# Performance work log

Measured on AMD Instinct MI355X. Metric: run time of the kernel, lower is better.

Reference implementation:

```python
import jax, jax.numpy as jnp
import numpy as np

B, T, E, H, D = 4, 2048, 1024, 16, 64  # batch, seq(block_size), n_embed, num_heads, hidden_dim


def setup_inputs() -> dict:
    key = jax.random.key(0)
    ks = jax.random.split(key, 10)
    s_in = 1.0 / np.sqrt(E)
    return {
        "x": jax.random.normal(ks[0], (B, T, E), dtype=jnp.float32),
        "Wq": jax.random.normal(ks[1], (H, E, D), dtype=jnp.float32) * s_in,
        "bq": jnp.zeros((H, D), dtype=jnp.float32),
        "Wk": jax.random.normal(ks[2], (H, E, D), dtype=jnp.float32) * s_in,
        "bk": jnp.zeros((H, D), dtype=jnp.float32),
        "Wv": jax.random.normal(ks[3], (H, E, D), dtype=jnp.float32) * s_in,
        "bv": jnp.zeros((H, D), dtype=jnp.float32),
        "Wp": jax.random.normal(ks[4], (E, E), dtype=jnp.float32) * s_in,
        "bp": jnp.zeros((E,), dtype=jnp.float32),
    }


def reference(x, Wq, bq, Wk, bk, Wv, bv, Wp, bp):
    # Batched equivalent of the per-head Python loop: each head h computes
    # causal scaled-dot-product attention with its own Q/K/V projections.
    q = jnp.einsum("bte,hed->bhtd", x, Wq) + bq[None, :, None, :]
    k = jnp.einsum("bte,hed->bhtd", x, Wk) + bk[None, :, None, :]
    v = jnp.einsum("bte,hed->bhtd", x, Wv) + bv[None, :, None, :]
    scale = 1.0 / jnp.sqrt(jnp.asarray(D, dtype=x.dtype))
    scores = jnp.einsum("bhtd,bhsd->bhts", q, k) * scale  # [B,H,T,T]
    causal = jnp.tril(jnp.ones((T, T), dtype=bool))
    scores = jnp.where(causal[None, None, :, :], scores, jnp.asarray(-jnp.inf, dtype=x.dtype))
    att = jax.nn.softmax(scores, axis=-1)
    head_out = jnp.einsum("bhts,bhsd->bhtd", att, v)  # [B,H,T,D]
    # concat heads along last dim: [B,T,H*D] == [B,T,E]
    cat = head_out.transpose(0, 2, 1, 3).reshape(B, T, H * D)
    out = cat @ Wp + bp  # final projection (dropout is identity in eval)
    return out
```

## Files before the change

kernel.cpp:

```cpp
#include <hip/hip_runtime.h>


typedef __attribute__((ext_vector_type(8))) __bf16 bf16x8;
typedef __attribute__((ext_vector_type(4))) float f32x4;
typedef __attribute__((ext_vector_type(16))) float f32x16;
typedef __attribute__((ext_vector_type(4))) unsigned int u32x4;
typedef __attribute__((ext_vector_type(2))) unsigned int u32x2;
typedef unsigned short u16;
typedef unsigned int u32;

#define DEV __device__ __forceinline__

#define QK_SCALE 0.18033688011112042f

DEV u16 f2bf(float f) {
  u32 u = __builtin_bit_cast(u32, f);
  u += 0x7fffu + ((u >> 16) & 1u);
  return (u16)(u >> 16);
}
DEV u32 pack2(float a, float b) { return (u32)f2bf(a) | ((u32)f2bf(b) << 16); }

DEV float exp2_hw(float x) { float r; asm("v_exp_f32 %0, %1" : "=v"(r) : "v"(x)); return r; }
DEV u32 cvtpk_bf16(float lo, float hi) {
  u32 r; asm("v_cvt_pk_bf16_f32 %0, %1, %2" : "=v"(r) : "v"(lo), "v"(hi)); return r;
}
DEV void pl32swap(u32& a, u32& b) { asm("v_permlane32_swap_b32 %0, %1" : "+v"(a), "+v"(b)); }
DEV float max3f(float a, float b, float c) {
  float r; asm("v_max3_f32 %0, %1, %2, %3" : "=v"(r) : "v"(a), "v"(b), "v"(c)); return r;
}

DEV f32x16 zero16() { f32x16 z;
#pragma unroll
  for (int i = 0; i < 16; i++) z[i] = 0.f;
  return z; }

__global__ __launch_bounds__(256) void prep_x_kernel(
    const float* __restrict__ x, const float* __restrict__ bq, const float* __restrict__ bk,
    const float* __restrict__ bv, u16* __restrict__ xbf, float* __restrict__ bqkv) {
  int gid = blockIdx.x * 256 + threadIdx.x;
  if (gid < 3072) {
    float v = (gid < 1024) ? bq[gid] * QK_SCALE : (gid < 2048 ? bk[gid - 1024] : bv[gid - 2048]);
    bqkv[gid] = v;
  }
  const float4* xv = (const float4*)x;
  float4 f0 = xv[(size_t)gid * 2];
  float4 f1 = xv[(size_t)gid * 2 + 1];
  u32x4 st;
  st.x = pack2(f0.x, f0.y); st.y = pack2(f0.z, f0.w);
  st.z = pack2(f1.x, f1.y); st.w = pack2(f1.z, f1.w);
  *(u32x4*)&xbf[(size_t)gid * 8] = st;
}

__global__ __launch_bounds__(256) void prep_w_kernel(
    const float* __restrict__ Wq, const float* __restrict__ Wk, const float* __restrict__ Wv,
    const float* __restrict__ Wp, u16* __restrict__ wqkvT, u16* __restrict__ wpT) {
  __shared__ float t[64][65];
  int bid = blockIdx.x, tid = threadIdx.x;
  int r0 = tid >> 6, c = tid & 63;
  if (bid < 768) {
    int p = bid >> 8, rem = bid & 255, h = rem >> 4, et = rem & 15;
    float sc = (p == 0) ? QK_SCALE : 1.0f;
    const float* src = (p == 0 ? Wq : (p == 1 ? Wk : Wv)) + ((size_t)h * 1024 + et * 64) * 64;
#pragma unroll
    for (int i = 0; i < 16; i++) { int e = r0 + i * 4; t[e][c] = src[(size_t)e * 64 + c]; }
    __syncthreads();
    u16* dst = wqkvT + ((size_t)p * 1024 + h * 64) * 1024 + et * 64;
#pragma unroll
    for (int i = 0; i < 16; i++) { int d = r0 + i * 4; dst[(size_t)d * 1024 + c] = f2bf(t[c][d] * sc); }
  } else {
    int b2 = bid - 768, rt = b2 >> 4, ct = b2 & 15;
#pragma unroll
    for (int i = 0; i < 16; i++) { int e = r0 + i * 4; t[e][c] = Wp[(size_t)(rt * 64 + e) * 1024 + ct * 64 + c]; }
    __syncthreads();
#pragma unroll
    for (int i = 0; i < 16; i++) { int f = r0 + i * 4; wpT[(size_t)(ct * 64 + f) * 1024 + rt * 64 + c] = f2bf(t[c][f]); }
  }
}

DEV void stage_tile(const u16* __restrict__ X, int row0, int k0, u16* lds, int tid) {
#pragma unroll
  for (int j = 0; j < 4; j++) {
    int ci = j * 256 + tid;
    int row = ci >> 3, slot = ci & 7;
    int srcslot = slot ^ (row & 7);
    const u16* gp = X + (size_t)(row0 + row) * 1024 + k0 + srcslot * 8;
    __builtin_amdgcn_global_load_lds((const __attribute__((address_space(1))) void*)gp,
                                     (__attribute__((address_space(3))) void*)(lds + ci * 8),
                                     16, 0, 0);
  }
}

__global__ __launch_bounds__(256) void gemm128_kernel(
    const u16* __restrict__ A, const u16* __restrict__ Bt, const float* __restrict__ bias,
    int tilesN, int mode, u16* __restrict__ Qb, u16* __restrict__ Kb, u16* __restrict__ VTb,
    float* __restrict__ outF) {
  __shared__ u16 As[128 * 64];
  __shared__ u16 Bs[128 * 64];
  int nwg = gridDim.x;
  int bid = blockIdx.x;
  int swz = (bid % 8) * (nwg / 8) + bid / 8;
  int bm = swz / tilesN, bn = swz % tilesN;
  int tid = threadIdx.x;
  int lane = tid & 63, wave = tid >> 6;
  int wm = wave >> 1, wn = wave & 1;
  int lr = lane & 15, lg = lane >> 4;

  f32x4 acc[4][4];
#pragma unroll
  for (int i = 0; i < 4; i++)
#pragma unroll
    for (int j = 0; j < 4; j++) acc[i][j] = f32x4{0.f, 0.f, 0.f, 0.f};

  for (int k0 = 0; k0 < 1024; k0 += 64) {
    stage_tile(A, bm * 128, k0, As, tid);
    stage_tile(Bt, bn * 128, k0, Bs, tid);
    __syncthreads();
#pragma unroll
    for (int kf = 0; kf < 2; kf++) {
      bf16x8 af[4], bfr[4];
#pragma unroll
      for (int i = 0; i < 4; i++) {
        int ra = wm * 64 + i * 16 + lr;
        af[i] = *(const bf16x8*)&As[ra * 64 + (((lg + kf * 4) ^ (ra & 7)) * 8)];
        int rb = wn * 64 + i * 16 + lr;
        bfr[i] = *(const bf16x8*)&Bs[rb * 64 + (((lg + kf * 4) ^ (rb & 7)) * 8)];
      }
      __builtin_amdgcn_s_setprio(1);
#pragma unroll
      for (int i = 0; i < 4; i++)
#pragma unroll
        for (int j = 0; j < 4; j++)
          acc[i][j] = __builtin_amdgcn_mfma_f32_16x16x32_bf16(af[i], bfr[j], acc[i][j], 0, 0, 0);
      __builtin_amdgcn_s_setprio(0);
    }
    __syncthreads();
  }

  int crow = bm * 128 + wm * 64;
  int ccol = bn * 128 + wn * 64;
  if (mode == 0) {
#pragma unroll
    for (int j = 0; j < 4; j++) {
      int col = ccol + j * 16 + lr;
      float bb = bias[col];
      int p = col >> 10, h = (col >> 6) & 15, d = col & 63;
#pragma unroll
      for (int i = 0; i < 4; i++) {
        int row0 = crow + i * 16 + lg * 4;
        int b_ = row0 >> 11, t0 = row0 & 2047;
        if (p == 2) {
          u32x2 pv;
          pv.x = pack2(acc[i][j][0] + bb, acc[i][j][1] + bb);
          pv.y = pack2(acc[i][j][2] + bb, acc[i][j][3] + bb);
          *(u32x2*)&VTb[((size_t)(b_ * 16 + h) * 64 + d) * 2048 + t0] = pv;
        } else {
          u16* dst = (p == 0 ? Qb : Kb);
#pragma unroll
          for (int r = 0; r < 4; r++)
            dst[((size_t)(b_ * 16 + h) * 2048 + (t0 + r)) * 64 + d] = f2bf(acc[i][j][r] + bb);
        }
      }
    }
  } else {
#pragma unroll
    for (int j = 0; j < 4; j++) {
      int col = ccol + j * 16 + lr;
      float bb = bias[col];
#pragma unroll
      for (int i = 0; i < 4; i++) {
        int row0 = crow + i * 16 + lg * 4;
#pragma unroll
        for (int r = 0; r < 4; r++)
          outF[(size_t)(row0 + r) * 1024 + col] = acc[i][j][r] + bb;
      }
    }
  }
}

DEV void stage_kv128(const u16* __restrict__ Kh, const u16* __restrict__ Vh, int kv0,
                     u16* Ksb, u16* Vsb, int tid) {
#pragma unroll
  for (int j = 0; j < 4; j++) {
    int ci = j * 128 + tid;
    int row = ci >> 3, slot = ci & 7;
    int ss = slot ^ (row & 7);
    __builtin_amdgcn_global_load_lds(
        (const __attribute__((address_space(1))) void*)(Kh + (size_t)(kv0 + row) * 64 + ss * 8),
        (__attribute__((address_space(3))) void*)(Ksb + ci * 8), 16, 0, 0);
    __builtin_amdgcn_global_load_lds(
        (const __attribute__((address_space(1))) void*)(Vh + (size_t)row * 2048 + kv0 + ss * 8),
        (__attribute__((address_space(3))) void*)(Vsb + ci * 8), 16, 0, 0);
  }
}

__global__ __launch_bounds__(128, 2) void attn_kernel(
    const u16* __restrict__ Qb, const u16* __restrict__ Kb, const u16* __restrict__ VTb,
    u16* __restrict__ cat) {
  __shared__ u16 Ks[2][64 * 64];
  __shared__ u16 Vs[2][64 * 64];
  int bid = blockIdx.x;
  int t = 31 - (bid >> 6);
  int bh = bid & 63;
  int b = bh >> 4, h = bh & 15;
  int tid = threadIdx.x, wave = tid >> 6, lane = tid & 63;
  int l31 = lane & 31, hi = lane >> 5;
  int qrow = t * 64 + wave * 32 + l31;

  const u16* Qh = Qb + (size_t)bh * 2048 * 64;
  const u16* Kh = Kb + (size_t)bh * 2048 * 64;
  const u16* Vh = VTb + (size_t)bh * 64 * 2048;

  bf16x8 qf[4];
#pragma unroll
  for (int ks = 0; ks < 4; ks++)
    qf[ks] = *(const bf16x8*)&Qh[(size_t)qrow * 64 + ks * 16 + hi * 8];

  u32 loff[4];
#pragma unroll
  for (int ks = 0; ks < 4; ks++)
    loff[ks] = (u32)(l31 * 128 + (((ks * 2 + hi) ^ (l31 & 7)) * 16));

  f32x16 o0 = zero16(), o1 = zero16();
  float m_run = -1e30f, l_run = 0.f;
  int iters = t + 1;

  stage_kv128(Kh, Vh, 0, Ks[0], Vs[0], tid);
  __syncthreads();
  int cur = 0;

  for (int kvt = 0; kvt < iters; ++kvt) {
    int kv0 = kvt * 64;
    if (kvt + 1 < iters) stage_kv128(Kh, Vh, kv0 + 64, Ks[cur ^ 1], Vs[cur ^ 1], tid);

    f32x16 s0 = zero16(), s1 = zero16();
    const char* kb = (const char*)&Ks[cur][0];
    __builtin_amdgcn_s_setprio(1);
#pragma unroll
    for (int ks = 0; ks < 4; ks++) {
      bf16x8 k0 = *(const bf16x8*)(kb + loff[ks]);
      bf16x8 k1 = *(const bf16x8*)(kb + loff[ks] + 4096);
      s0 = __builtin_amdgcn_mfma_f32_32x32x16_bf16(k0, qf[ks], s0, 0, 0, 0);
      s1 = __builtin_amdgcn_mfma_f32_32x32x16_bf16(k1, qf[ks], s1, 0, 0, 0);
    }
    __builtin_amdgcn_s_setprio(0);

    if (kvt == t) {
      int relh = qrow - kv0 - 4 * hi;
#pragma unroll
      for (int r = 0; r < 16; r++) {
        int off = (r & 3) + 8 * (r >> 2);
        s0[r] = (off > relh) ? -1e30f : s0[r];
        s1[r] = (off + 32 > relh) ? -1e30f : s1[r];
      }
    }

    float ta = max3f(s0[0], s0[1], s0[2]);
    float tb = max3f(s0[4], s0[5], s0[6]);
    float tc = max3f(s0[8], s0[9], s0[10]);
    float td = max3f(s0[12], s0[13], s0[14]);
    ta = max3f(ta, s0[3], s1[0]);
    tb = max3f(tb, s0[7], s1[4]);
    tc = max3f(tc, s0[11], s1[8]);
    td = max3f(td, s0[15], s1[12]);
    ta = max3f(ta, s1[1], s1[2]);
    tb = max3f(tb, s1[5], s1[6]);
    tc = max3f(tc, s1[9], s1[10]);
    td = max3f(td, s1[13], s1[14]);
    ta = max3f(ta, s1[3], tb);
    tc = max3f(tc, s1[7], td);
    float tmax = max3f(ta, tc, s1[11]);
    tmax = fmaxf(tmax, s1[15]);
    tmax = fmaxf(tmax, __shfl_xor(tmax, 32));
    float corr = 1.f;
    if (!__all(tmax <= m_run + 8.f)) {
      float m_new = fmaxf(m_run, tmax);
      corr = exp2_hw(m_run - m_new);
      o0 = o0 * corr;
      o1 = o1 * corr;
      m_run = m_new;
    }
    float t0 = 0.f, t1 = 0.f, t2 = 0.f, t3 = 0.f;
#pragma unroll
    for (int j = 0; j < 4; j++) {
      float p00 = exp2_hw(s0[j * 4 + 0] - m_run); s0[j * 4 + 0] = p00; t0 += p00;
      float p01 = exp2_hw(s0[j * 4 + 1] - m_run); s0[j * 4 + 1] = p01; t1 += p01;
      float p02 = exp2_hw(s0[j * 4 + 2] - m_run); s0[j * 4 + 2] = p02; t2 += p02;
      float p03 = exp2_hw(s0[j * 4 + 3] - m_run); s0[j * 4 + 3] = p03; t3 += p03;
      float p10 = exp2_hw(s1[j * 4 + 0] - m_run); s1[j * 4 + 0] = p10; t0 += p10;
      float p11 = exp2_hw(s1[j * 4 + 1] - m_run); s1[j * 4 + 1] = p11; t1 += p11;
      float p12 = exp2_hw(s1[j * 4 + 2] - m_run); s1[j * 4 + 2] = p12; t2 += p12;
      float p13 = exp2_hw(s1[j * 4 + 3] - m_run); s1[j * 4 + 3] = p13; t3 += p13;
    }
    float ts = (t0 + t1) + (t2 + t3);
    ts += __shfl_xor(ts, 32);
    l_run = l_run * corr + ts;

    const char* vb = (const char*)&Vs[cur][0];
    __builtin_amdgcn_s_setprio(1);
#pragma unroll
    for (int ks = 0; ks < 4; ks++) {
      const f32x16& sb = (ks < 2) ? s0 : s1;
      int g2 = (ks & 1) * 8;
      u32 a  = cvtpk_bf16(sb[g2 + 0], sb[g2 + 1]);
      u32 c  = cvtpk_bf16(sb[g2 + 2], sb[g2 + 3]);
      u32 bb = cvtpk_bf16(sb[g2 + 4], sb[g2 + 5]);
      u32 d  = cvtpk_bf16(sb[g2 + 6], sb[g2 + 7]);
      pl32swap(a, bb);
      pl32swap(c, d);
      u32x4 wv; wv.x = a; wv.y = c; wv.z = bb; wv.w = d;
      bf16x8 pf = __builtin_bit_cast(bf16x8, wv);
      bf16x8 v0 = *(const bf16x8*)(vb + loff[ks]);
      bf16x8 v1 = *(const bf16x8*)(vb + loff[ks] + 4096);
      o0 = __builtin_amdgcn_mfma_f32_32x32x16_bf16(v0, pf, o0, 0, 0, 0);
      o1 = __builtin_amdgcn_mfma_f32_32x32x16_bf16(v1, pf, o1, 0, 0, 0);
    }
    __builtin_amdgcn_s_setprio(0);

    __syncthreads();
    cur ^= 1;
  }

  float li = 1.0f / l_run;
#pragma unroll
  for (int m = 0; m < 8; m++) {
    int dbase = 2 * (m & 1) + 8 * (m >> 1) + 4 * hi;
    u32 w0 = cvtpk_bf16(o0[2 * m] * li, o0[2 * m + 1] * li);
    u32 w1 = cvtpk_bf16(o1[2 * m] * li, o1[2 * m + 1] * li);
    *(u32*)&cat[(size_t)(b * 2048 + qrow) * 1024 + h * 64 + dbase] = w0;
    *(u32*)&cat[(size_t)(b * 2048 + qrow) * 1024 + h * 64 + 32 + dbase] = w1;
  }
}

extern "C" void kernel_launch(void* const* d_in, const int* in_sizes, int n_in,
                              void* d_out, int out_size, void* d_ws, size_t ws_size,
                              hipStream_t stream) {
  const float* x  = (const float*)d_in[0];
  const float* Wq = (const float*)d_in[1];
  const float* bq = (const float*)d_in[2];
  const float* Wk = (const float*)d_in[3];
  const float* bk = (const float*)d_in[4];
  const float* Wv = (const float*)d_in[5];
  const float* bv = (const float*)d_in[6];
  const float* Wp = (const float*)d_in[7];
  const float* bp = (const float*)d_in[8];

  char* w = (char*)d_ws;
  u16* xbf    = (u16*)w;                 w += (size_t)8192 * 1024 * 2;
  u16* wqkvT  = (u16*)w;                 w += (size_t)3072 * 1024 * 2;
  u16* wpT    = (u16*)w;                 w += (size_t)1024 * 1024 * 2;
  float* bqkv = (float*)w;               w += (size_t)3072 * 4;
  u16* Qb     = (u16*)w;                 w += (size_t)64 * 2048 * 64 * 2;
  u16* Kb     = (u16*)w;                 w += (size_t)64 * 2048 * 64 * 2;
  u16* VTb    = (u16*)w;                 w += (size_t)64 * 64 * 2048 * 2;
  u16* cat    = (u16*)w;                 w += (size_t)8192 * 1024 * 2;

  prep_x_kernel<<<4096, 256, 0, stream>>>(x, bq, bk, bv, xbf, bqkv);
  prep_w_kernel<<<1024, 256, 0, stream>>>(Wq, Wk, Wv, Wp, wqkvT, wpT);
  gemm128_kernel<<<1536, 256, 0, stream>>>(xbf, wqkvT, bqkv, 24, 0, Qb, Kb, VTb, nullptr);
  attn_kernel<<<2048, 128, 0, stream>>>(Qb, Kb, VTb, cat);
  gemm128_kernel<<<512, 256, 0, stream>>>(cat, wpT, bp, 8, 1, nullptr, nullptr, nullptr, (float*)d_out);
}
```

Baseline: 167.4 us.

## Replace 128x128 GEMM with 256x128 triple-buffered pipelined GEMM using 8 waves

Rewrites the projection GEMM kernel to use 256x128 output tiles with 512 threads and a three-slot LDS ring buffer. Global-to-LDS loads for step k+2 are interleaved with MFMA quadrants of the current step, and explicit waitcnt and sched barriers control ordering. The goal is to hide global load latency and cut per-step barrier stalls, and the larger tile raises operand reuse. In exchange the kernel uses more LDS and registers, issues more barriers per iteration, and launches half as many workgroups, which may hurt occupancy or load balance.

Measured after the change: 166.0 us. No clear change (-0.8%).

```diff
diff --git a/kernel.cpp b/kernel.cpp
--- a/kernel.cpp
+++ b/kernel.cpp
@@ -33,6 +33,15 @@
 #pragma unroll
   for (int i = 0; i < 16; i++) z[i] = 0.f;
   return z; }
+
+DEV void gll16(const u16* g, u16* l) {
+  __builtin_amdgcn_global_load_lds((const __attribute__((address_space(1))) void*)g,
+                                   (__attribute__((address_space(3))) void*)l, 16, 0, 0);
+}
+
+#define SCHEDB() __builtin_amdgcn_sched_barrier(0)
+#define SBAR()   do { __builtin_amdgcn_s_barrier(); SCHEDB(); } while (0)
+#define LGKM0()  do { asm volatile("s_waitcnt lgkmcnt(0)" ::: "memory"); SCHEDB(); } while (0)
 
 __global__ __launch_bounds__(256) void prep_x_kernel(
     const float* __restrict__ x, const float* __restrict__ bq, const float* __restrict__ bk,
@@ -77,25 +86,33 @@
   }
 }
 
-DEV void stage_tile(const u16* __restrict__ X, int row0, int k0, u16* lds, int tid) {
-#pragma unroll
-  for (int j = 0; j < 4; j++) {
-    int ci = j * 256 + tid;
-    int row = ci >> 3, slot = ci & 7;
-    int srcslot = slot ^ (row & 7);
-    const u16* gp = X + (size_t)(row0 + row) * 1024 + k0 + srcslot * 8;
-    __builtin_amdgcn_global_load_lds((const __attribute__((address_space(1))) void*)gp,
-                                     (__attribute__((address_space(3))) void*)(lds + ci * 8),
-                                     16, 0, 0);
-  }
-}
-
-__global__ __launch_bounds__(256) void gemm128_kernel(
+#define SLOT_U16 24576
+
+DEV void stageA_unit(const u16* __restrict__ Asrc, int row0, int k0, int h, u16* An, int tid) {
+#pragma unroll
+  for (int jj = 0; jj < 2; jj++) {
+    int idx = jj * 512 + tid;
+    int row = h * 128 + (idx >> 3), slot = idx & 7;
+    int ss = slot ^ (row & 7);
+    gll16(Asrc + (size_t)(row0 + row) * 1024 + k0 + ss * 8, An + (size_t)row * 64 + slot * 8);
+  }
+}
+DEV void stageB_unit(const u16* __restrict__ Bsrc, int row0, int k0, int h, u16* Bn, int tid) {
+  int idx = tid;
+  int row = h * 64 + (idx >> 3), slot = idx & 7;
+  int ss = slot ^ (row & 7);
+  gll16(Bsrc + (size_t)(row0 + row) * 1024 + k0 + ss * 8, Bn + (size_t)row * 64 + slot * 8);
+}
+
+DEV bf16x8 ldsAB(const u16* base, int row, int kk, int lg) {
+  return *(const bf16x8*)&base[row * 64 + (((lg + kk * 4) ^ (row & 7)) * 8)];
+}
+
+__global__ __launch_bounds__(512, 2) void gemm256_kernel(
     const u16* __restrict__ A, const u16* __restrict__ Bt, const float* __restrict__ bias,
     int tilesN, int mode, u16* __restrict__ Qb, u16* __restrict__ Kb, u16* __restrict__ VTb,
     float* __restrict__ outF) {
-  __shared__ u16 As[128 * 64];
-  __shared__ u16 Bs[128 * 64];
+  __shared__ u16 lds[3 * SLOT_U16];
   int nwg = gridDim.x;
   int bid = blockIdx.x;
   int swz = (bid % 8) * (nwg / 8) + bid / 8;
@@ -104,6 +121,8 @@
   int lane = tid & 63, wave = tid >> 6;
   int wm = wave >> 1, wn = wave & 1;
   int lr = lane & 15, lg = lane >> 4;
+  int aRow0 = bm * 256, bRow0 = bn * 128;
+  int ar = wm * 64, br = wn * 64;
 
   f32x4 acc[4][4];
 #pragma unroll
@@ -111,33 +130,107 @@
 #pragma unroll
     for (int j = 0; j < 4; j++) acc[i][j] = f32x4{0.f, 0.f, 0.f, 0.f};
 
-  for (int k0 = 0; k0 < 1024; k0 += 64) {
-    stage_tile(A, bm * 128, k0, As, tid);
-    stage_tile(Bt, bn * 128, k0, Bs, tid);
-    __syncthreads();
-#pragma unroll
-    for (int kf = 0; kf < 2; kf++) {
-      bf16x8 af[4], bfr[4];
-#pragma unroll
-      for (int i = 0; i < 4; i++) {
-        int ra = wm * 64 + i * 16 + lr;
-        af[i] = *(const bf16x8*)&As[ra * 64 + (((lg + kf * 4) ^ (ra & 7)) * 8)];
-        int rb = wn * 64 + i * 16 + lr;
-        bfr[i] = *(const bf16x8*)&Bs[rb * 64 + (((lg + kf * 4) ^ (rb & 7)) * 8)];
-      }
-      __builtin_amdgcn_s_setprio(1);
-#pragma unroll
-      for (int i = 0; i < 4; i++)
-#pragma unroll
-        for (int j = 0; j < 4; j++)
-          acc[i][j] = __builtin_amdgcn_mfma_f32_16x16x32_bf16(af[i], bfr[j], acc[i][j], 0, 0, 0);
-      __builtin_amdgcn_s_setprio(0);
-    }
-    __syncthreads();
-  }
-
-  int crow = bm * 128 + wm * 64;
-  int ccol = bn * 128 + wn * 64;
+#pragma unroll
+  for (int pt = 0; pt < 2; pt++) {
+    u16* As = lds + pt * SLOT_U16;
+    stageA_unit(A, aRow0, pt * 64, 0, As, tid);
+    stageA_unit(A, aRow0, pt * 64, 1, As, tid);
+    stageB_unit(Bt, bRow0, pt * 64, 0, As + 16384, tid);
+    stageB_unit(Bt, bRow0, pt * 64, 1, As + 16384, tid);
+  }
+  asm volatile("s_waitcnt vmcnt(6)" ::: "memory");
+  SCHEDB();
+  SBAR();
+
+  int rs = 0;
+  for (int t = 0; t < 16; ++t) {
+    u16* Ac = lds + rs * SLOT_U16;
+    u16* Bc = Ac + 16384;
+    int ws = rs + 2; if (ws >= 3) ws -= 3;
+    u16* An = lds + ws * SLOT_U16;
+    u16* Bn = An + 16384;
+    int k2 = (t + 2) * 64;
+    bool st = (t + 2) < 16;
+
+    bf16x8 aLo[2][2], bLo[2][2];
+#pragma unroll
+    for (int i = 0; i < 2; i++)
+#pragma unroll
+      for (int kk = 0; kk < 2; kk++) aLo[i][kk] = ldsAB(Ac, ar + i * 16 + lr, kk, lg);
+#pragma unroll
+    for (int j = 0; j < 2; j++)
+#pragma unroll
+      for (int kk = 0; kk < 2; kk++) bLo[j][kk] = ldsAB(Bc, br + j * 16 + lr, kk, lg);
+    if (st) stageA_unit(A, aRow0, k2, 0, An, tid);
+    SBAR(); LGKM0();
+    __builtin_amdgcn_s_setprio(1);
+#pragma unroll
+    for (int kk = 0; kk < 2; kk++)
+#pragma unroll
+      for (int i = 0; i < 2; i++)
+#pragma unroll
+        for (int j = 0; j < 2; j++)
+          acc[i][j] = __builtin_amdgcn_mfma_f32_16x16x32_bf16(aLo[i][kk], bLo[j][kk], acc[i][j], 0, 0, 0);
+    __builtin_amdgcn_s_setprio(0);
+    SBAR();
+
+    bf16x8 bHi[2][2];
+#pragma unroll
+    for (int j = 0; j < 2; j++)
+#pragma unroll
+      for (int kk = 0; kk < 2; kk++) bHi[j][kk] = ldsAB(Bc, br + 32 + j * 16 + lr, kk, lg);
+    if (st) stageB_unit(Bt, bRow0, k2, 0, Bn, tid);
+    SBAR(); LGKM0();
+    __builtin_amdgcn_s_setprio(1);
+#pragma unroll
+    for (int kk = 0; kk < 2; kk++)
+#pragma unroll
+      for (int i = 0; i < 2; i++)
+#pragma unroll
+        for (int j = 0; j < 2; j++)
+          acc[i][j + 2] = __builtin_amdgcn_mfma_f32_16x16x32_bf16(aLo[i][kk], bHi[j][kk], acc[i][j + 2], 0, 0, 0);
+    __builtin_amdgcn_s_setprio(0);
+    SBAR();
+
+    bf16x8 aHi[2][2];
+#pragma unroll
+    for (int i = 0; i < 2; i++)
+#pragma unroll
+      for (int kk = 0; kk < 2; kk++) aHi[i][kk] = ldsAB(Ac, ar + 32 + i * 16 + lr, kk, lg);
+    if (st) stageA_unit(A, aRow0, k2, 1, An, tid);
+    SBAR(); LGKM0();
+    __builtin_amdgcn_s_setprio(1);
+#pragma unroll
+    for (int kk = 0; kk < 2; kk++)
+#pragma unroll
+      for (int i = 0; i < 2; i++)
+#pragma unroll
+        for (int j = 0; j < 2; j++)
+          acc[i + 2][j + 2] = __builtin_amdgcn_mfma_f32_16x16x32_bf16(aHi[i][kk], bHi[j][kk], acc[i + 2][j + 2], 0, 0, 0);
+    __builtin_amdgcn_s_setprio(0);
+    SBAR();
+
+    if (st) stageB_unit(Bt, bRow0, k2, 1, Bn, tid);
+    SBAR();
+    __builtin_amdgcn_s_setprio(1);
+#pragma unroll
+    for (int kk = 0; kk < 2; kk++)
+#pragma unroll
+      for (int i = 0; i < 2; i++)
+#pragma unroll
+        for (int j = 0; j < 2; j++)
+          acc[i + 2][j] = __builtin_amdgcn_mfma_f32_16x16x32_bf16(aHi[i][kk], bLo[j][kk], acc[i + 2][j], 0, 0, 0);
+    __builtin_amdgcn_s_setprio(0);
+    if (t < 14) { asm volatile("s_waitcnt vmcnt(6)" ::: "memory"); }
+    else if (t == 14) { asm volatile("s_waitcnt vmcnt(0)" ::: "memory"); }
+    SCHEDB();
+    SBAR();
+
+    rs = (rs == 2) ? 0 : rs + 1;
+  }
+
+  int crow = aRow0 + wm * 64;
+  int ccol = bRow0 + wn * 64;
   if (mode == 0) {
 #pragma unroll
     for (int j = 0; j < 4; j++) {
@@ -356,7 +449,7 @@
 
   prep_x_kernel<<<4096, 256, 0, stream>>>(x, bq, bk, bv, xbf, bqkv);
   prep_w_kernel<<<1024, 256, 0, stream>>>(Wq, Wk, Wv, Wp, wqkvT, wpT);
-  gemm128_kernel<<<1536, 256, 0, stream>>>(xbf, wqkvT, bqkv, 24, 0, Qb, Kb, VTb, nullptr);
+  gemm256_kernel<<<768, 512, 0, stream>>>(xbf, wqkvT, bqkv, 24, 0, Qb, Kb, VTb, nullptr);
   attn_kernel<<<2048, 128, 0, stream>>>(Qb, Kb, VTb, cat);
-  gemm128_kernel<<<512, 256, 0, stream>>>(cat, wpT, bp, 8, 1, nullptr, nullptr, nullptr, (float*)d_out);
-}
+  gemm256_kernel<<<256, 512, 0, stream>>>(cat, wpT, bp, 8, 1, nullptr, nullptr, nullptr, (float*)d_out);
+}
```
